# Performance work log

Measured on AMD Instinct MI355X. Metric: run time of the kernel, lower is better.

The kernel has to match this reference:

```python
import jax, jax.numpy as jnp
import numpy as np

NUM_NODES = 1_000_000
IN_FEATS = 128
N_HIDDEN = 256
N_CLASSES = 47
# block sizes: fanouts [15,10,5], batch 1024
N_SRC = [1081344, 67584, 6144]
N_DST = [67584, 6144, 1024]
N_EDGE = [1013760, 61440, 5120]


def setup_inputs() -> dict:
    key = jax.random.key(0)
    ks = jax.random.split(key, 16)
    inp = {}
    inp["emb_table"] = jax.random.normal(ks[0], (NUM_NODES, IN_FEATS), dtype=jnp.float32)
    inp["input_nodes"] = jax.random.randint(ks[1], (N_SRC[0],), 0, NUM_NODES)
    for l in range(3):
        inp[f"src{l}"] = jax.random.randint(ks[2 + 2 * l], (N_EDGE[l],), 0, N_SRC[l])
        inp[f"dst{l}"] = jax.random.randint(ks[3 + 2 * l], (N_EDGE[l],), 0, N_DST[l])
    dims = [(IN_FEATS, N_HIDDEN), (N_HIDDEN, N_HIDDEN), (N_HIDDEN, N_CLASSES)]
    for l, (din, dout) in enumerate(dims):
        s = 1.0 / np.sqrt(din)
        inp[f"Wself{l}"] = jax.random.uniform(ks[8 + 2 * l], (din, dout), minval=-s, maxval=s, dtype=jnp.float32)
        inp[f"Wneigh{l}"] = jax.random.uniform(ks[9 + 2 * l], (din, dout), minval=-s, maxval=s, dtype=jnp.float32)
        inp[f"b{l}"] = jnp.zeros((dout,), dtype=jnp.float32)
    return inp


def _sage_layer(h, src, dst, n_dst, Wself, Wneigh, b):
    # DGL SAGEConv 'mean': out = fc_self(h_dst) + fc_neigh(mean_{u in N(v)} h_u) + bias
    h_dst = h[:n_dst]
    msg = h[src]                                   # [E, din] irregular gather
    agg = jax.ops.segment_sum(msg, dst, num_segments=n_dst)
    deg = jax.ops.segment_sum(jnp.ones((src.shape[0],), h.dtype), dst, num_segments=n_dst)
    agg = agg / jnp.maximum(deg, 1.0)[:, None]     # segment mean (0-degree -> 0)
    return h_dst @ Wself + agg @ Wneigh + b


def reference(emb_table, Wself0, Wneigh0, b0, Wself1, Wneigh1, b1, Wself2, Wneigh2, b2,
              input_nodes, src0, dst0, src1, dst1, src2, dst2):
    h = emb_table[input_nodes]                     # embedding lookup
    params = [(src0, dst0, N_DST[0], Wself0, Wneigh0, b0),
              (src1, dst1, N_DST[1], Wself1, Wneigh1, b1),
              (src2, dst2, N_DST[2], Wself2, Wneigh2, b2)]
    for l, (s, d, nd, Ws, Wn, b) in enumerate(params):
        h = _sage_layer(h, s, d, nd, Ws, Wn, b)
        if l != 2:
            h = jax.nn.relu(h)                     # dropout p=0 -> identity
    return h
```

## Files before the change

kernel.cpp:

```cpp
#include <hip/hip_runtime.h>
#include <cstdint>
#include <cstddef>

#define NDST0 67584
#define NDST1 6144
#define NDST2 1024
#define NEDGE0 1013760
#define NEDGE1 61440
#define NEDGE2 5120
#define F0 128
#define F1 256
#define NCLS 47

__global__ __launch_bounds__(256) void hist_kernel(
    const int* __restrict__ dst, int nedge, int* __restrict__ cnt)
{
    int e = blockIdx.x * 256 + threadIdx.x;
    const int stride = gridDim.x * 256;
    for (; e < nedge; e += stride)
        atomicAdd(&cnt[dst[e]], 1);
}

__global__ __launch_bounds__(1024) void scan_kernel(
    const int* __restrict__ cnt, int n,
    int* __restrict__ rs, int* __restrict__ work)
{
    __shared__ int sums[1024];
    const int tid = threadIdx.x;
    const int L = (n + 1023) >> 10;
    const int lo = tid * L;
    const int hi = (lo + L < n) ? (lo + L) : n;
    int s = 0;
    for (int i = lo; i < hi; ++i) s += cnt[i];
    sums[tid] = s;
    __syncthreads();
    int v = s;
    for (int off = 1; off < 1024; off <<= 1) {
        int t = (tid >= off) ? sums[tid - off] : 0;
        __syncthreads();
        v += t;
        sums[tid] = v;
        __syncthreads();
    }
    int run = v - s;
    for (int i = lo; i < hi; ++i) {
        rs[i] = run;
        work[i] = run;
        run += cnt[i];
    }
    if (tid == 1023) rs[n] = run;
}

__global__ __launch_bounds__(256) void fill_kernel(
    const int* __restrict__ src, const int* __restrict__ dst,
    const int* __restrict__ idx, int nedge,
    int* __restrict__ work, int* __restrict__ esrc)
{
    int e = blockIdx.x * 256 + threadIdx.x;
    if (e >= nedge) return;
    const int s = src[e];
    const int row = idx ? idx[s] : s;
    const int p = atomicAdd(&work[dst[e]], 1);
    esrc[p] = row;
}

__global__ __launch_bounds__(256) void gather_kernel(
    const float* __restrict__ table, const int* __restrict__ esrc,
    const int* __restrict__ rs, const int* __restrict__ cnt,
    int nd, int feat, int lshift, float* __restrict__ agg)
{
    const int lanes = 1 << lshift;
    const int gpb = 256 >> lshift;
    const int d = blockIdx.x * gpb + ((int)threadIdx.x >> lshift);
    if (d >= nd) return;
    const int lane = (int)threadIdx.x & (lanes - 1);
    const int start = rs[d];
    const int c = cnt[d];
    const float* tb = table + (size_t)lane * 4;
    float4 acc = make_float4(0.f, 0.f, 0.f, 0.f);
    int i = 0;
    for (; i + 1 < c; i += 2) {
        const int r0 = esrc[start + i];
        const int r1 = esrc[start + i + 1];
        const float4 v0 = *(const float4*)(tb + (size_t)r0 * feat);
        const float4 v1 = *(const float4*)(tb + (size_t)r1 * feat);
        acc.x += v0.x + v1.x; acc.y += v0.y + v1.y;
        acc.z += v0.z + v1.z; acc.w += v0.w + v1.w;
    }
    if (i < c) {
        const int r0 = esrc[start + i];
        const float4 v0 = *(const float4*)(tb + (size_t)r0 * feat);
        acc.x += v0.x; acc.y += v0.y; acc.z += v0.z; acc.w += v0.w;
    }
    const float sc = 1.0f / fmaxf((float)c, 1.0f);
    float4 o = make_float4(acc.x * sc, acc.y * sc, acc.z * sc, acc.w * sc);
    *(float4*)(agg + (size_t)d * feat + lane * 4) = o;
}

__global__ __launch_bounds__(256) void sage_gemm(
    const float* __restrict__ table, const int* __restrict__ idx,
    const float* __restrict__ agg,
    const float* __restrict__ Wself, const float* __restrict__ Wneigh,
    const float* __restrict__ bias, float* __restrict__ out,
    int dout, int din, int do_relu)
{
    __shared__ float As[16][68];
    __shared__ float Bs[16][68];

    const int tid = threadIdx.x;
    const int m0 = blockIdx.x * 64;
    const int n0 = blockIdx.y * 64;

    const int tm = tid >> 4;
    const int tn = tid & 15;

    const int lrow = tid >> 2;
    const int lk4  = (tid & 3) << 2;
    const int bkk  = tid >> 4;
    const int bn4  = (tid & 15) << 2;

    const int gmA = m0 + lrow;
    const long rowA = idx ? (long)idx[gmA] : (long)gmA;
    const float* tptr = table + rowA * din;
    const float* aptr = agg + (size_t)gmA * din;

    float acc[4][4] = {};

    const int K2 = 2 * din;
    for (int k0 = 0; k0 < K2; k0 += 16) {
        const bool self_phase = (k0 < din);
        float4 av;
        if (self_phase) {
            av = *(const float4*)(tptr + k0 + lk4);
        } else {
            av = *(const float4*)(aptr + (k0 - din) + lk4);
        }
        const float* W = self_phase ? Wself : Wneigh;
        const int kb = (self_phase ? k0 : (k0 - din)) + bkk;
        const float* wp = W + (size_t)kb * dout + n0 + bn4;
        float bv0, bv1, bv2, bv3;
        if (n0 + bn4 + 3 < dout) {
            const float4 w4 = *(const float4*)wp;
            bv0 = w4.x; bv1 = w4.y; bv2 = w4.z; bv3 = w4.w;
        } else {
            bv0 = (n0 + bn4 + 0 < dout) ? wp[0] : 0.0f;
            bv1 = (n0 + bn4 + 1 < dout) ? wp[1] : 0.0f;
            bv2 = (n0 + bn4 + 2 < dout) ? wp[2] : 0.0f;
            bv3 = (n0 + bn4 + 3 < dout) ? wp[3] : 0.0f;
        }

        __syncthreads();
        As[lk4 + 0][lrow] = av.x;
        As[lk4 + 1][lrow] = av.y;
        As[lk4 + 2][lrow] = av.z;
        As[lk4 + 3][lrow] = av.w;
        Bs[bkk][bn4 + 0] = bv0;
        Bs[bkk][bn4 + 1] = bv1;
        Bs[bkk][bn4 + 2] = bv2;
        Bs[bkk][bn4 + 3] = bv3;
        __syncthreads();

        #pragma unroll
        for (int kk = 0; kk < 16; ++kk) {
            const float4 a4 = *(const float4*)&As[kk][tm << 2];
            const float4 b4 = *(const float4*)&Bs[kk][tn << 2];
            const float a_[4] = {a4.x, a4.y, a4.z, a4.w};
            const float b_[4] = {b4.x, b4.y, b4.z, b4.w};
            #pragma unroll
            for (int i = 0; i < 4; ++i)
                #pragma unroll
                for (int j = 0; j < 4; ++j)
                    acc[i][j] += a_[i] * b_[j];
        }
    }

    #pragma unroll
    for (int i = 0; i < 4; ++i) {
        const size_t gm = m0 + (tm << 2) + i;
        #pragma unroll
        for (int j = 0; j < 4; ++j) {
            const int gn = n0 + (tn << 2) + j;
            if (gn < dout) {
                float v = acc[i][j] + bias[gn];
                if (do_relu) v = fmaxf(v, 0.0f);
                out[gm * dout + gn] = v;
            }
        }
    }
}

extern "C" void kernel_launch(void* const* d_in, const int* in_sizes, int n_in,
                              void* d_out, int out_size, void* d_ws, size_t ws_size,
                              hipStream_t stream)
{
    const float* emb         = (const float*)d_in[0];
    const int*   input_nodes = (const int*)d_in[1];
    const int*   src0 = (const int*)d_in[2];
    const int*   dst0 = (const int*)d_in[3];
    const int*   src1 = (const int*)d_in[4];
    const int*   dst1 = (const int*)d_in[5];
    const int*   src2 = (const int*)d_in[6];
    const int*   dst2 = (const int*)d_in[7];
    const float* Ws0 = (const float*)d_in[8];
    const float* Wn0 = (const float*)d_in[9];
    const float* b0  = (const float*)d_in[10];
    const float* Ws1 = (const float*)d_in[11];
    const float* Wn1 = (const float*)d_in[12];
    const float* b1  = (const float*)d_in[13];
    const float* Ws2 = (const float*)d_in[14];
    const float* Wn2 = (const float*)d_in[15];
    const float* b2  = (const float*)d_in[16];
    float* out = (float*)d_out;

    float* ws   = (float*)d_ws;
    float* agg0 = ws;
    float* agg1 = agg0 + (size_t)NDST0 * F0;
    float* agg2 = agg1 + (size_t)NDST1 * F1;
    float* h1   = agg2 + (size_t)NDST2 * F1;
    float* h2   = h1 + (size_t)NDST0 * F1;

    int* ip    = (int*)(h2 + (size_t)NDST1 * F1);
    int* cnt0  = ip;               ip += NDST0;
    int* cnt1  = ip;               ip += NDST1;
    int* cnt2  = ip;               ip += NDST2;
    const size_t zero_bytes = (size_t)(NDST0 + NDST1 + NDST2) * sizeof(int);
    int* rs0   = ip;               ip += NDST0 + 1;
    int* work0 = ip;               ip += NDST0;
    int* rs1   = ip;               ip += NDST1 + 1;
    int* work1 = ip;               ip += NDST1;
    int* rs2   = ip;               ip += NDST2 + 1;
    int* work2 = ip;               ip += NDST2;
    int* esrc0 = ip;               ip += NEDGE0;
    int* esrc1 = ip;               ip += NEDGE1;
    int* esrc2 = ip;               ip += NEDGE2;

    hipMemsetAsync(cnt0, 0, zero_bytes, stream);

    hist_kernel<<<1024, 256, 0, stream>>>(dst0, NEDGE0, cnt0);
    scan_kernel<<<1, 1024, 0, stream>>>(cnt0, NDST0, rs0, work0);
    fill_kernel<<<(NEDGE0 + 255) / 256, 256, 0, stream>>>(src0, dst0, input_nodes, NEDGE0, work0, esrc0);
    gather_kernel<<<(NDST0 + 7) / 8, 256, 0, stream>>>(emb, esrc0, rs0, cnt0, NDST0, F0, 5, agg0);
    sage_gemm<<<dim3(NDST0 / 64, 256 / 64), 256, 0, stream>>>(
        emb, input_nodes, agg0, Ws0, Wn0, b0, h1, 256, F0, 1);

    hist_kernel<<<256, 256, 0, stream>>>(dst1, NEDGE1, cnt1);
    scan_kernel<<<1, 1024, 0, stream>>>(cnt1, NDST1, rs1, work1);
    fill_kernel<<<(NEDGE1 + 255) / 256, 256, 0, stream>>>(src1, dst1, nullptr, NEDGE1, work1, esrc1);
    gather_kernel<<<(NDST1 + 3) / 4, 256, 0, stream>>>(h1, esrc1, rs1, cnt1, NDST1, F1, 6, agg1);
    sage_gemm<<<dim3(NDST1 / 64, 256 / 64), 256, 0, stream>>>(
        h1, nullptr, agg1, Ws1, Wn1, b1, h2, 256, F1, 1);

    hist_kernel<<<64, 256, 0, stream>>>(dst2, NEDGE2, cnt2);
    scan_kernel<<<1, 1024, 0, stream>>>(cnt2, NDST2, rs2, work2);
    fill_kernel<<<(NEDGE2 + 255) / 256, 256, 0, stream>>>(src2, dst2, nullptr, NEDGE2, work2, esrc2);
    gather_kernel<<<(NDST2 + 3) / 4, 256, 0, stream>>>(h2, esrc2, rs2, cnt2, NDST2, F1, 6, agg2);
    sage_gemm<<<dim3(NDST2 / 64, 1), 256, 0, stream>>>(
        h2, nullptr, agg2, Ws2, Wn2, b2, out, NCLS, F1, 0);
}
```

Measured before the change: 1.144 ms.

## Switch SAGE GEMMs to bf16 MFMA with bf16 intermediate activations

```diff
diff --git a/kernel.cpp b/kernel.cpp
--- a/kernel.cpp
+++ b/kernel.cpp
@@ -11,6 +11,27 @@
 #define F0 128
 #define F1 256
 #define NCLS 47
+
+typedef unsigned short ushort_t;
+typedef __attribute__((ext_vector_type(8))) short short8;
+typedef __attribute__((ext_vector_type(4))) float floatx4;
+
+__device__ __forceinline__ ushort_t f2bf(float f) {
+    union { float f; unsigned u; } v; v.f = f;
+    unsigned r = v.u + 0x7fffu + ((v.u >> 16) & 1u);
+    return (ushort_t)(r >> 16);
+}
+__device__ __forceinline__ float bf2f(ushort_t u) {
+    union { unsigned u; float f; } v; v.u = ((unsigned)u) << 16;
+    return v.f;
+}
+
+__device__ __forceinline__ void async_copy16(ushort_t* lds, const ushort_t* g) {
+    __builtin_amdgcn_global_load_lds(
+        (const __attribute__((address_space(1))) unsigned*)(g),
+        (__attribute__((address_space(3))) unsigned*)(lds),
+        16, 0, 0);
+}
 
 __global__ __launch_bounds__(256) void hist_kernel(
     const int* __restrict__ dst, int nedge, int* __restrict__ cnt)
@@ -64,10 +85,10 @@
     esrc[p] = row;
 }
 
-__global__ __launch_bounds__(256) void gather_kernel(
+__global__ __launch_bounds__(256) void gather_f32(
     const float* __restrict__ table, const int* __restrict__ esrc,
     const int* __restrict__ rs, const int* __restrict__ cnt,
-    int nd, int feat, int lshift, float* __restrict__ agg)
+    int nd, int feat, int lshift, ushort_t* __restrict__ agg)
 {
     const int lanes = 1 << lshift;
     const int gpb = 256 >> lshift;
@@ -93,97 +114,143 @@
         acc.x += v0.x; acc.y += v0.y; acc.z += v0.z; acc.w += v0.w;
     }
     const float sc = 1.0f / fmaxf((float)c, 1.0f);
-    float4 o = make_float4(acc.x * sc, acc.y * sc, acc.z * sc, acc.w * sc);
-    *(float4*)(agg + (size_t)d * feat + lane * 4) = o;
-}
-
-__global__ __launch_bounds__(256) void sage_gemm(
-    const float* __restrict__ table, const int* __restrict__ idx,
-    const float* __restrict__ agg,
-    const float* __restrict__ Wself, const float* __restrict__ Wneigh,
-    const float* __restrict__ bias, float* __restrict__ out,
-    int dout, int din, int do_relu)
-{
-    __shared__ float As[16][68];
-    __shared__ float Bs[16][68];
-
-    const int tid = threadIdx.x;
-    const int m0 = blockIdx.x * 64;
-    const int n0 = blockIdx.y * 64;
-
-    const int tm = tid >> 4;
-    const int tn = tid & 15;
-
-    const int lrow = tid >> 2;
-    const int lk4  = (tid & 3) << 2;
-    const int bkk  = tid >> 4;
-    const int bn4  = (tid & 15) << 2;
-
-    const int gmA = m0 + lrow;
-    const long rowA = idx ? (long)idx[gmA] : (long)gmA;
-    const float* tptr = table + rowA * din;
-    const float* aptr = agg + (size_t)gmA * din;
-
-    float acc[4][4] = {};
-
+    ushort4 o;
+    o.x = f2bf(acc.x * sc); o.y = f2bf(acc.y * sc);
+    o.z = f2bf(acc.z * sc); o.w = f2bf(acc.w * sc);
+    *(ushort4*)(agg + (size_t)d * feat + lane * 4) = o;
+}
+
+__global__ __launch_bounds__(256) void gather_bf16(
+    const ushort_t* __restrict__ table, const int* __restrict__ esrc,
+    const int* __restrict__ rs, const int* __restrict__ cnt,
+    int nd, int feat, int lshift, ushort_t* __restrict__ agg)
+{
+    const int lanes = 1 << lshift;
+    const int gpb = 256 >> lshift;
+    const int d = blockIdx.x * gpb + ((int)threadIdx.x >> lshift);
+    if (d >= nd) return;
+    const int lane = (int)threadIdx.x & (lanes - 1);
+    const int start = rs[d];
+    const int c = cnt[d];
+    const ushort_t* tb = table + (size_t)lane * 4;
+    float ax = 0.f, ay = 0.f, az = 0.f, aw = 0.f;
+    for (int i = 0; i < c; ++i) {
+        const int r0 = esrc[start + i];
+        const ushort4 v = *(const ushort4*)(tb + (size_t)r0 * feat);
+        ax += bf2f(v.x); ay += bf2f(v.y); az += bf2f(v.z); aw += bf2f(v.w);
+    }
+    const float sc = 1.0f / fmaxf((float)c, 1.0f);
+    ushort4 o;
+    o.x = f2bf(ax * sc); o.y = f2bf(ay * sc);
+    o.z = f2bf(az * sc); o.w = f2bf(aw * sc);
+    *(ushort4*)(agg + (size_t)d * feat + lane * 4) = o;
+}
+
+__global__ __launch_bounds__(256) void sel_convert(
+    const float* __restrict__ emb, const int* __restrict__ idx,
+    int m_total, int feat, ushort_t* __restrict__ outb)
+{
+    const int q = blockIdx.x * 256 + threadIdx.x;
+    const int qpr = feat >> 2;
+    if (q >= m_total * qpr) return;
+    const int m = q / qpr;
+    const int c = q - m * qpr;
+    const int row = idx[m];
+    const float4 v = *(const float4*)(emb + (size_t)row * feat + c * 4);
+    ushort4 o;
+    o.x = f2bf(v.x); o.y = f2bf(v.y); o.z = f2bf(v.z); o.w = f2bf(v.w);
+    *(ushort4*)(outb + (size_t)m * feat + c * 4) = o;
+}
+
+__global__ __launch_bounds__(256) void wprep_kernel(
+    const float* __restrict__ Ws, const float* __restrict__ Wn,
+    int din, int dout, int npad, ushort_t* __restrict__ Bt)
+{
+    const int id = blockIdx.x * 256 + threadIdx.x;
     const int K2 = 2 * din;
-    for (int k0 = 0; k0 < K2; k0 += 16) {
-        const bool self_phase = (k0 < din);
-        float4 av;
-        if (self_phase) {
-            av = *(const float4*)(tptr + k0 + lk4);
-        } else {
-            av = *(const float4*)(aptr + (k0 - din) + lk4);
+    if (id >= npad * K2) return;
+    const int n = id / K2;
+    const int k2 = id - n * K2;
+    float v = 0.f;
+    if (n < dout)
+        v = (k2 < din) ? Ws[(size_t)k2 * dout + n] : Wn[(size_t)(k2 - din) * dout + n];
+    Bt[id] = f2bf(v);
+}
+
+__global__ __launch_bounds__(256) void mfma_gemm(
+    const ushort_t* __restrict__ Aself, const ushort_t* __restrict__ Aneigh,
+    const ushort_t* __restrict__ Bt, const float* __restrict__ bias,
+    void* __restrict__ outp, int din, int dout, int out_bf16, int do_relu)
+{
+    __shared__ ushort_t As[128 * 32];
+    __shared__ ushort_t Bs[128 * 32];
+
+    const int tid  = threadIdx.x;
+    const int wave = tid >> 6;
+    const int lane = tid & 63;
+    const int m0 = blockIdx.x * 128;
+    const int n0 = blockIdx.y * 128;
+    const int wm = (wave & 1) * 64;
+    const int wn = (wave >> 1) * 64;
+
+    const int arow = lane >> 2;
+    const int achk = (lane & 3) * 8;
+
+    const int K2 = 2 * din;
+
+    floatx4 acc[4][4];
+    const floatx4 zero = {0.f, 0.f, 0.f, 0.f};
+    #pragma unroll
+    for (int i = 0; i < 4; ++i)
+        #pragma unroll
+        for (int j = 0; j < 4; ++j) acc[i][j] = zero;
+
+    const int fr = lane & 15;
+    const int fq = (lane >> 4) * 8;
+
+    for (int k0 = 0; k0 < K2; k0 += 32) {
+        const ushort_t* Abase = (k0 < din) ? (Aself + k0) : (Aneigh + (k0 - din));
+        #pragma unroll
+        for (int i = 0; i < 2; ++i) {
+            const int rg = (wave * 2 + i) * 16 + arow;
+            async_copy16(&As[rg * 32 + achk],
+                         Abase + (size_t)(m0 + rg) * din + achk);
+            async_copy16(&Bs[rg * 32 + achk],
+                         Bt + (size_t)(n0 + rg) * K2 + k0 + achk);
         }
-        const float* W = self_phase ? Wself : Wneigh;
-        const int kb = (self_phase ? k0 : (k0 - din)) + bkk;
-        const float* wp = W + (size_t)kb * dout + n0 + bn4;
-        float bv0, bv1, bv2, bv3;
-        if (n0 + bn4 + 3 < dout) {
-            const float4 w4 = *(const float4*)wp;
-            bv0 = w4.x; bv1 = w4.y; bv2 = w4.z; bv3 = w4.w;
-        } else {
-            bv0 = (n0 + bn4 + 0 < dout) ? wp[0] : 0.0f;
-            bv1 = (n0 + bn4 + 1 < dout) ? wp[1] : 0.0f;
-            bv2 = (n0 + bn4 + 2 < dout) ? wp[2] : 0.0f;
-            bv3 = (n0 + bn4 + 3 < dout) ? wp[3] : 0.0f;
+        __syncthreads();
+
+        short8 a[4], b[4];
+        #pragma unroll
+        for (int f = 0; f < 4; ++f) {
+            a[f] = *(const short8*)&As[(wm + f * 16 + fr) * 32 + fq];
+            b[f] = *(const short8*)&Bs[(wn + f * 16 + fr) * 32 + fq];
         }
-
+        #pragma unroll
+        for (int fm = 0; fm < 4; ++fm)
+            #pragma unroll
+            for (int fn = 0; fn < 4; ++fn)
+                acc[fm][fn] = __builtin_amdgcn_mfma_f32_16x16x32_bf16(
+                    a[fm], b[fn], acc[fm][fn], 0, 0, 0);
         __syncthreads();
-        As[lk4 + 0][lrow] = av.x;
-        As[lk4 + 1][lrow] = av.y;
-        As[lk4 + 2][lrow] = av.z;
-        As[lk4 + 3][lrow] = av.w;
-        Bs[bkk][bn4 + 0] = bv0;
-        Bs[bkk][bn4 + 1] = bv1;
-        Bs[bkk][bn4 + 2] = bv2;
-        Bs[bkk][bn4 + 3] = bv3;
-        __syncthreads();
-
-        #pragma unroll
-        for (int kk = 0; kk < 16; ++kk) {
-            const float4 a4 = *(const float4*)&As[kk][tm << 2];
-            const float4 b4 = *(const float4*)&Bs[kk][tn << 2];
-            const float a_[4] = {a4.x, a4.y, a4.z, a4.w};
-            const float b_[4] = {b4.x, b4.y, b4.z, b4.w};
+    }
+
+    const int erow = (lane >> 4) * 4;
+    const int ecol = lane & 15;
+    #pragma unroll
+    for (int fn = 0; fn < 4; ++fn) {
+        const int gn = n0 + wn + fn * 16 + ecol;
+        if (gn >= dout) continue;
+        const float bv = bias[gn];
+        #pragma unroll
+        for (int fm = 0; fm < 4; ++fm) {
             #pragma unroll
-            for (int i = 0; i < 4; ++i)
-                #pragma unroll
-                for (int j = 0; j < 4; ++j)
-                    acc[i][j] += a_[i] * b_[j];
-        }
-    }
-
-    #pragma unroll
-    for (int i = 0; i < 4; ++i) {
-        const size_t gm = m0 + (tm << 2) + i;
-        #pragma unroll
-        for (int j = 0; j < 4; ++j) {
-            const int gn = n0 + (tn << 2) + j;
-            if (gn < dout) {
-                float v = acc[i][j] + bias[gn];
-                if (do_relu) v = fmaxf(v, 0.0f);
-                out[gm * dout + gn] = v;
+            for (int r = 0; r < 4; ++r) {
+                const size_t gm = m0 + wm + fm * 16 + erow + r;
+                float v = acc[fm][fn][r] + bv;
+                if (do_relu) v = fmaxf(v, 0.f);
+                if (out_bf16) ((ushort_t*)outp)[gm * dout + gn] = f2bf(v);
+                else          ((float*)outp)[gm * dout + gn] = v;
             }
         }
     }
@@ -212,48 +279,59 @@
     const float* b2  = (const float*)d_in[16];
     float* out = (float*)d_out;
 
-    float* ws   = (float*)d_ws;
-    float* agg0 = ws;
-    float* agg1 = agg0 + (size_t)NDST0 * F0;
-    float* agg2 = agg1 + (size_t)NDST1 * F1;
-    float* h1   = agg2 + (size_t)NDST2 * F1;
-    float* h2   = h1 + (size_t)NDST0 * F1;
-
-    int* ip    = (int*)(h2 + (size_t)NDST1 * F1);
-    int* cnt0  = ip;               ip += NDST0;
-    int* cnt1  = ip;               ip += NDST1;
-    int* cnt2  = ip;               ip += NDST2;
+    ushort_t* us     = (ushort_t*)d_ws;
+    ushort_t* embsel = us;
+    ushort_t* agg0   = embsel + (size_t)NDST0 * F0;
+    ushort_t* h1     = agg0 + (size_t)NDST0 * F0;
+    ushort_t* agg1   = h1 + (size_t)NDST0 * F1;
+    ushort_t* h2     = agg1 + (size_t)NDST1 * F1;
+    ushort_t* agg2   = h2 + (size_t)NDST1 * F1;
+    ushort_t* Bt0    = agg2 + (size_t)NDST2 * F1;
+    ushort_t* Bt1    = Bt0 + 256 * 256;
+    ushort_t* Bt2    = Bt1 + 256 * 512;
+
+    int* ip   = (int*)(Bt2 + 128 * 512);
+    int* cnt0 = ip;  ip += NDST0;
+    int* cnt1 = ip;  ip += NDST1;
+    int* cnt2 = ip;  ip += NDST2;
     const size_t zero_bytes = (size_t)(NDST0 + NDST1 + NDST2) * sizeof(int);
-    int* rs0   = ip;               ip += NDST0 + 1;
-    int* work0 = ip;               ip += NDST0;
-    int* rs1   = ip;               ip += NDST1 + 1;
-    int* work1 = ip;               ip += NDST1;
-    int* rs2   = ip;               ip += NDST2 + 1;
-    int* work2 = ip;               ip += NDST2;
-    int* esrc0 = ip;               ip += NEDGE0;
-    int* esrc1 = ip;               ip += NEDGE1;
-    int* esrc2 = ip;               ip += NEDGE2;
+    int* rs0   = ip; ip += NDST0 + 1;
+    int* work0 = ip; ip += NDST0;
+    int* rs1   = ip; ip += NDST1 + 1;
+    int* work1 = ip; ip += NDST1;
+    int* rs2   = ip; ip += NDST2 + 1;
+    int* work2 = ip; ip += NDST2;
+    int* esrc0 = ip; ip += NEDGE0;
+    int* esrc1 = ip; ip += NEDGE1;
+    int* esrc2 = ip; ip += NEDGE2;
 
     hipMemsetAsync(cnt0, 0, zero_bytes, stream);
+
+    wprep_kernel<<<(256 * 256 + 255) / 256, 256, 0, stream>>>(Ws0, Wn0, F0, 256, 256, Bt0);
+    wprep_kernel<<<(256 * 512 + 255) / 256, 256, 0, stream>>>(Ws1, Wn1, F1, 256, 256, Bt1);
+    wprep_kernel<<<(128 * 512 + 255) / 256, 256, 0, stream>>>(Ws2, Wn2, F1, NCLS, 128, Bt2);
+
+    sel_convert<<<(NDST0 * (F0 / 4) + 255) / 256, 256, 0, stream>>>(
+        emb, input_nodes, NDST0, F0, embsel);
 
     hist_kernel<<<1024, 256, 0, stream>>>(dst0, NEDGE0, cnt0);
     scan_kernel<<<1, 1024, 0, stream>>>(cnt0, NDST0, rs0, work0);
     fill_kernel<<<(NEDGE0 + 255) / 256, 256, 0, stream>>>(src0, dst0, input_nodes, NEDGE0, work0, esrc0);
-    gather_kernel<<<(NDST0 + 7) / 8, 256, 0, stream>>>(emb, esrc0, rs0, cnt0, NDST0, F0, 5, agg0);
-    sage_gemm<<<dim3(NDST0 / 64, 256 / 64), 256, 0, stream>>>(
-        emb, input_nodes, agg0, Ws0, Wn0, b0, h1, 256, F0, 1);
+    gather_f32<<<NDST0 / 8, 256, 0, stream>>>(emb, esrc0, rs0, cnt0, NDST0, F0, 5, agg0);
+    mfma_gemm<<<dim3(NDST0 / 128, 256 / 128), 256, 0, stream>>>(
+        embsel, agg0, Bt0, b0, h1, F0, 256, 1, 1);
 
     hist_kernel<<<256, 256, 0, stream>>>(dst1, NEDGE1, cnt1);
     scan_kernel<<<1, 1024, 0, stream>>>(cnt1, NDST1, rs1, work1);
     fill_kernel<<<(NEDGE1 + 255) / 256, 256, 0, stream>>>(src1, dst1, nullptr, NEDGE1, work1, esrc1);
-    gather_kernel<<<(NDST1 + 3) / 4, 256, 0, stream>>>(h1, esrc1, rs1, cnt1, NDST1, F1, 6, agg1);
-    sage_gemm<<<dim3(NDST1 / 64, 256 / 64), 256, 0, stream>>>(
-        h1, nullptr, agg1, Ws1, Wn1, b1, h2, 256, F1, 1);
+    gather_bf16<<<NDST1 / 4, 256, 0, stream>>>(h1, esrc1, rs1, cnt1, NDST1, F1, 6, agg1);
+    mfma_gemm<<<dim3(NDST1 / 128, 256 / 128), 256, 0, stream>>>(
+        h1, agg1, Bt1, b1, h2, F1, 256, 1, 1);
 
     hist_kernel<<<64, 256, 0, stream>>>(dst2, NEDGE2, cnt2);
     scan_kernel<<<1, 1024, 0, stream>>>(cnt2, NDST2, rs2, work2);
     fill_kernel<<<(NEDGE2 + 255) / 256, 256, 0, stream>>>(src2, dst2, nullptr, NEDGE2, work2, esrc2);
-    gather_kernel<<<(NDST2 + 3) / 4, 256, 0, stream>>>(h2, esrc2, rs2, cnt2, NDST2, F1, 6, agg2);
-    sage_gemm<<<dim3(NDST2 / 64, 1), 256, 0, stream>>>(
-        h2, nullptr, agg2, Ws2, Wn2, b2, out, NCLS, F1, 0);
-}
+    gather_bf16<<<NDST2 / 4, 256, 0, stream>>>(h2, esrc2, rs2, cnt2, NDST2, F1, 6, agg2);
+    mfma_gemm<<<dim3(NDST2 / 128, 1), 256, 0, stream>>>(
+        h2, agg2, Bt2, b2, out, F1, NCLS, 0, 0);
+}
```

Measured after the change: 1.026 ms. 1.12x faster.
